# Kernel optimization log

Hardware: AMD Instinct MI355X
Metric: run time of the kernel (lower is better)

The kernel has to match this reference:

```python
import jax, jax.numpy as jnp
import numpy as np

B, W, F = 64, 128, 64          # batch, window (node feat dim), n_features (nodes)
H, OUTW = 4, 128               # num_heads, out window size
NEG_SLOPE = 0.2                # LeakyReLU negative slope (alpha)


def setup_inputs() -> dict:
    key = jax.random.key(0)
    ks = jax.random.split(key, 6)
    scale_in = 1.0 / np.sqrt(W)
    scale_a = 1.0 / np.sqrt(OUTW)
    return {
        "x": jax.random.normal(ks[0], (B, W, F), dtype=jnp.float32),
        "W_src": jax.random.normal(ks[1], (H * OUTW, W), dtype=jnp.float32) * scale_in,
        "b_src": jnp.zeros((H * OUTW,), dtype=jnp.float32),
        "W_dst": jax.random.normal(ks[2], (H * OUTW, W), dtype=jnp.float32) * scale_in,
        "b_dst": jnp.zeros((H * OUTW,), dtype=jnp.float32),
        "attn": jax.random.normal(ks[3], (H, OUTW), dtype=jnp.float32) * scale_a,
    }


def reference(x, W_src, b_src, W_dst, b_dst, attn):
    # x: [B, W, F] -> node features nf: [B, F, W] (F nodes, W-dim features)
    nf = jnp.transpose(x, (0, 2, 1))
    b, f, w = nf.shape
    h, outw = attn.shape
    # GATv2 separate source/destination projections (share_weights=False)
    fs = (nf @ W_src.T + b_src).reshape(b, f, h, outw)  # [B, F, H, outW]
    fd = (nf @ W_dst.T + b_dst).reshape(b, f, h, outw)
    # additive score over complete graph with self-loops: e[b,i,j,h,d]
    s = fs[:, :, None, :, :] + fd[:, None, :, :, :]      # [B, src, dst, H, outW]
    e = jnp.where(s >= 0, s, NEG_SLOPE * s)              # LeakyReLU
    scores = jnp.einsum('bijhd,hd->bhij', e, attn)       # [B, H, src, dst]
    # edge softmax: normalize over incoming edges (sources) per destination
    a = jax.nn.softmax(scores, axis=2)
    # weighted scatter-sum aggregation at destinations
    out = jnp.einsum('bhij,bihd->bjhd', a, fs)           # [B, F, H, outW]
    out = out.mean(axis=2)                               # mean over heads -> [B, F, outW]
    return jnp.transpose(out, (0, 2, 1))                 # [B, outW, F]
```

## Files before the change

### kernel.cpp

```cpp
#include <hip/hip_runtime.h>
#include <math.h>

#define BB 64
#define WW 128
#define FF 64
#define HH 4
#define OW 128


struct GemmRegion {
    float xq[64 * 68];
    float wq[2 * 128 * 68];
};
struct AttnRegion {
    float fsl[FF * 132];
    float fdl[FF * 132];
    float stT[FF * 68];
    float st2[FF * 68];
    float A6[OW], B4[OW];
    float redm[4 * 64];
    float invl[64];
    float xfer[256 * 36];
};
union SMem { GemmRegion g; AttnRegion a; };

__global__ void __launch_bounds__(512)
__attribute__((amdgpu_waves_per_eu(2, 2)))
gat_fused(
    const float* __restrict__ x,
    const float* __restrict__ Wsrc,
    const float* __restrict__ bsrc,
    const float* __restrict__ Wdst,
    const float* __restrict__ bdst,
    const float* __restrict__ attn,
    float* __restrict__ out)
{
    __shared__ __align__(16) SMem sm;
    __shared__ float bl[2 * 128];

    const int bx = blockIdx.x;
    const int h  = bx & 3;
    const int b  = bx >> 2;
    const int t  = threadIdx.x;

    const int m  = (t >> 7) & 1;
    const int ig = (t >> 4) & 7;
    const int dg = t & 15;
    const int i0 = ig * 8;

    if (t < 256) bl[t] = (t & 128 ? bdst : bsrc)[h * 128 + (t & 127)];

    float acc[8][8] = {};

    for (int kh = 0; kh < 2; ++kh) {
        if (kh) __syncthreads();
        #pragma unroll
        for (int p = 0; p < 2; ++p) {
            const int idx = p * 512 + t;
            const int k = idx >> 4, iq = idx & 15;
            *(float4*)&sm.g.xq[k * 68 + iq * 4] =
                *(const float4*)(x + ((size_t)b * WW + kh * 64 + k) * FF + iq * 4);
        }
        #pragma unroll
        for (int p = 0; p < 8; ++p) {
            const int idx = p * 512 + t;
            const int mm = idx >> 11, d = (idx >> 4) & 127, q = idx & 15;
            *(float4*)&sm.g.wq[(mm * 128 + d) * 68 + q * 4] =
                *(const float4*)((mm ? Wdst : Wsrc)
                                 + (size_t)(h * 128 + d) * WW + kh * 64 + q * 4);
        }
        __syncthreads();

        if (t < 256) {
            #pragma unroll 1
            for (int k0 = 0; k0 < 64; k0 += 4) {
                float4 wv[8];
                #pragma unroll
                for (int e = 0; e < 8; ++e)
                    wv[e] = *(const float4*)&sm.g.wq[(m * 128 + dg + 16 * e) * 68 + k0];
                #pragma unroll
                for (int kk = 0; kk < 4; ++kk) {
                    const float4 xa = *(const float4*)&sm.g.xq[(k0 + kk) * 68 + i0];
                    const float4 xb = *(const float4*)&sm.g.xq[(k0 + kk) * 68 + i0 + 4];
                    #pragma unroll
                    for (int e = 0; e < 8; ++e) {
                        const float wf = ((const float*)&wv[e])[kk];
                        acc[0][e] = fmaf(xa.x, wf, acc[0][e]);
                        acc[1][e] = fmaf(xa.y, wf, acc[1][e]);
                        acc[2][e] = fmaf(xa.z, wf, acc[2][e]);
                        acc[3][e] = fmaf(xa.w, wf, acc[3][e]);
                        acc[4][e] = fmaf(xb.x, wf, acc[4][e]);
                        acc[5][e] = fmaf(xb.y, wf, acc[5][e]);
                        acc[6][e] = fmaf(xb.z, wf, acc[6][e]);
                        acc[7][e] = fmaf(xb.w, wf, acc[7][e]);
                    }
                }
            }
        }
    }
    __syncthreads();

    if (t < 256) {
        float* dst = m ? sm.a.fdl : sm.a.fsl;
        #pragma unroll
        for (int e = 0; e < 8; ++e) {
            const int d = dg + 16 * e;
            const float bv = bl[m * 128 + d];
            #pragma unroll
            for (int ii = 0; ii < 8; ++ii)
                dst[(i0 + ii) * 132 + d] = acc[ii][e] + bv;
        }
    }
    if (t < 128) {
        const float av = attn[h * OW + t];
        sm.a.A6[t] = 0.6f * av;
        sm.a.B4[t] = 0.4f * av;
    }
    __syncthreads();

    if (t < 256) {
        const int i = t & 63, sel = t >> 6;
        const float* src = (sel < 2 ? sm.a.fsl : sm.a.fdl) + i * 132 + (sel & 1) * 64;
        const float* a6  = sm.a.A6 + (sel & 1) * 64;
        float s = 0.0f;
        #pragma unroll
        for (int c = 0; c < 16; ++c) {
            float4 fv = *(const float4*)&src[c * 4];
            float4 av = *(const float4*)&a6[c * 4];
            s = fmaf(fv.x, av.x, fmaf(fv.y, av.y, fmaf(fv.z, av.z, fmaf(fv.w, av.w, s))));
        }
        sm.a.redm[sel * 64 + i] = s;
    }
    __syncthreads();

    {
        const int dh  = t >> 8;
        const int rem = t & 255;
        const int iT  = rem & 15;
        const int j0D = (rem >> 4) * 4;
        float4 scq[4];
        scq[0] = scq[1] = scq[2] = scq[3] = float4{0.f, 0.f, 0.f, 0.f};
        const int cBase = dh * 16;
        #pragma unroll 4
        for (int c = 0; c < 16; ++c) {
            const int dd0 = (cBase + c) * 4;
            const float4 b4 = *(const float4*)&sm.a.B4[dd0];
            float4 fdv[4];
            #pragma unroll
            for (int jj = 0; jj < 4; ++jj)
                fdv[jj] = *(const float4*)&sm.a.fdl[(j0D + jj) * 132 + dd0];
            #pragma unroll
            for (int ii = 0; ii < 4; ++ii) {
                const float4 fsv =
                    *(const float4*)&sm.a.fsl[(iT + 16 * ii) * 132 + dd0];
                float* sc = (float*)&scq[ii];
                #pragma unroll
                for (int jj = 0; jj < 4; ++jj) {
                    float r = sc[jj];
                    r = fmaf(b4.x, fabsf(fsv.x + fdv[jj].x), r);
                    r = fmaf(b4.y, fabsf(fsv.y + fdv[jj].y), r);
                    r = fmaf(b4.z, fabsf(fsv.z + fdv[jj].z), r);
                    r = fmaf(b4.w, fabsf(fsv.w + fdv[jj].w), r);
                    sc[jj] = r;
                }
            }
        }
        if (dh) {
            #pragma unroll
            for (int ii = 0; ii < 4; ++ii)
                *(float4*)&sm.a.st2[(iT + 16 * ii) * 68 + j0D] = scq[ii];
        }
        __syncthreads();
        if (!dh) {
            float cdj[4];
            #pragma unroll
            for (int jj = 0; jj < 4; ++jj)
                cdj[jj] = sm.a.redm[128 + j0D + jj] + sm.a.redm[192 + j0D + jj];
            #pragma unroll
            for (int ii = 0; ii < 4; ++ii) {
                const int i = iT + 16 * ii;
                const float4 p2 = *(const float4*)&sm.a.st2[i * 68 + j0D];
                const float csl = sm.a.redm[i] + sm.a.redm[64 + i];
                const float* sc = (const float*)&scq[ii];
                const float* pp = (const float*)&p2;
                #pragma unroll
                for (int jj = 0; jj < 4; ++jj)
                    sm.a.stT[(j0D + jj) * 68 + i] = sc[jj] + pp[jj] + csl + cdj[jj];
            }
        }
    }
    __syncthreads();

    if (t < 64) {
        const int j = t;
        float* row = &sm.a.stT[j * 68];
        float4 rv[16];
        float mx = -3.0e38f;
        #pragma unroll
        for (int q = 0; q < 16; ++q) {
            rv[q] = *(const float4*)&row[q * 4];
            mx = fmaxf(mx, fmaxf(fmaxf(rv[q].x, rv[q].y), fmaxf(rv[q].z, rv[q].w)));
        }
        float s = 0.0f;
        #pragma unroll
        for (int q = 0; q < 16; ++q) {
            float4 e;
            e.x = __expf(rv[q].x - mx);
            e.y = __expf(rv[q].y - mx);
            e.z = __expf(rv[q].z - mx);
            e.w = __expf(rv[q].w - mx);
            s += e.x + e.y + e.z + e.w;
            *(float4*)&row[q * 4] = e;
        }
        sm.a.invl[j] = 0.25f / s;
    }
    __syncthreads();

    {
        const int ih  = t >> 8;
        const int rem = t & 255;
        const int jT  = rem & 15;
        const int dgF = rem >> 4;
        const int dF  = dgF * 4;
        const int iBase = ih * 32;

        float ag[4][8] = {};
        #pragma unroll 2
        for (int i2 = 0; i2 < 32; i2 += 4) {
            float4 pq[4];
            #pragma unroll
            for (int jj = 0; jj < 4; ++jj)
                pq[jj] = *(const float4*)&sm.a.stT[(jT + 16 * jj) * 68 + iBase + i2];
            #pragma unroll
            for (int u = 0; u < 4; ++u) {
                const int i = iBase + i2 + u;
                const float4 f0 = *(const float4*)&sm.a.fsl[i * 132 + dF];
                const float4 f1 = *(const float4*)&sm.a.fsl[i * 132 + dF + 64];
                #pragma unroll
                for (int jj = 0; jj < 4; ++jj) {
                    const float p = ((const float*)&pq[jj])[u];
                    ag[jj][0] = fmaf(p, f0.x, ag[jj][0]);
                    ag[jj][1] = fmaf(p, f0.y, ag[jj][1]);
                    ag[jj][2] = fmaf(p, f0.z, ag[jj][2]);
                    ag[jj][3] = fmaf(p, f0.w, ag[jj][3]);
                    ag[jj][4] = fmaf(p, f1.x, ag[jj][4]);
                    ag[jj][5] = fmaf(p, f1.y, ag[jj][5]);
                    ag[jj][6] = fmaf(p, f1.z, ag[jj][6]);
                    ag[jj][7] = fmaf(p, f1.w, ag[jj][7]);
                }
            }
        }

        if (ih) {
            #pragma unroll
            for (int jj = 0; jj < 4; ++jj) {
                float4 a0 = {ag[jj][0], ag[jj][1], ag[jj][2], ag[jj][3]};
                float4 a1 = {ag[jj][4], ag[jj][5], ag[jj][6], ag[jj][7]};
                *(float4*)&sm.a.xfer[rem * 36 + jj * 8]     = a0;
                *(float4*)&sm.a.xfer[rem * 36 + jj * 8 + 4] = a1;
            }
        }
        __syncthreads();
        if (!ih) {
            float* ob = out + (size_t)b * OW * FF;
            #pragma unroll
            for (int jj = 0; jj < 4; ++jj) {
                const float4 a0 = *(const float4*)&sm.a.xfer[rem * 36 + jj * 8];
                const float4 a1 = *(const float4*)&sm.a.xfer[rem * 36 + jj * 8 + 4];
                const float iv = sm.a.invl[jT + 16 * jj];
                const int j = jT + 16 * jj;
                atomicAdd(ob + (size_t)(dF + 0) * FF + j, (ag[jj][0] + a0.x) * iv);
                atomicAdd(ob + (size_t)(dF + 1) * FF + j, (ag[jj][1] + a0.y) * iv);
                atomicAdd(ob + (size_t)(dF + 2) * FF + j, (ag[jj][2] + a0.z) * iv);
                atomicAdd(ob + (size_t)(dF + 3) * FF + j, (ag[jj][3] + a0.w) * iv);
                atomicAdd(ob + (size_t)(dF + 64) * FF + j, (ag[jj][4] + a1.x) * iv);
                atomicAdd(ob + (size_t)(dF + 65) * FF + j, (ag[jj][5] + a1.y) * iv);
                atomicAdd(ob + (size_t)(dF + 66) * FF + j, (ag[jj][6] + a1.z) * iv);
                atomicAdd(ob + (size_t)(dF + 67) * FF + j, (ag[jj][7] + a1.w) * iv);
            }
        }
    }
}

extern "C" void kernel_launch(void* const* d_in, const int* in_sizes, int n_in,
                              void* d_out, int out_size, void* d_ws, size_t ws_size,
                              hipStream_t stream) {
    const float* x    = (const float*)d_in[0];
    const float* Wsrc = (const float*)d_in[1];
    const float* bsrc = (const float*)d_in[2];
    const float* Wdst = (const float*)d_in[3];
    const float* bdst = (const float*)d_in[4];
    const float* attn = (const float*)d_in[5];

    hipMemsetAsync(d_out, 0, (size_t)out_size, stream);
    gat_fused<<<BB * HH, 512, 0, stream>>>(x, Wsrc, bsrc, Wdst, bdst, attn,
                                           (float*)d_out);
}
```

Measured before the change: 102.6 us.

## Spread projection GEMM across all 512 threads and read x directly from global

```diff
diff --git a/kernel.cpp b/kernel.cpp
--- a/kernel.cpp
+++ b/kernel.cpp
@@ -9,7 +9,6 @@
 
 
 struct GemmRegion {
-    float xq[64 * 68];
     float wq[2 * 128 * 68];
 };
 struct AttnRegion {
@@ -43,24 +42,19 @@
     const int b  = bx >> 2;
     const int t  = threadIdx.x;
 
-    const int m  = (t >> 7) & 1;
-    const int ig = (t >> 4) & 7;
+    const int m  = t >> 8;
+    const int ig = (t >> 4) & 15;
     const int dg = t & 15;
-    const int i0 = ig * 8;
+    const int i0 = ig * 4;
 
     if (t < 256) bl[t] = (t & 128 ? bdst : bsrc)[h * 128 + (t & 127)];
 
-    float acc[8][8] = {};
+    const float* xb = x + (size_t)b * (WW * FF);
+
+    float acc[4][8] = {};
 
     for (int kh = 0; kh < 2; ++kh) {
         if (kh) __syncthreads();
-        #pragma unroll
-        for (int p = 0; p < 2; ++p) {
-            const int idx = p * 512 + t;
-            const int k = idx >> 4, iq = idx & 15;
-            *(float4*)&sm.g.xq[k * 68 + iq * 4] =
-                *(const float4*)(x + ((size_t)b * WW + kh * 64 + k) * FF + iq * 4);
-        }
         #pragma unroll
         for (int p = 0; p < 8; ++p) {
             const int idx = p * 512 + t;
@@ -71,43 +65,37 @@
         }
         __syncthreads();
 
-        if (t < 256) {
-            #pragma unroll 1
-            for (int k0 = 0; k0 < 64; k0 += 4) {
-                float4 wv[8];
-                #pragma unroll
-                for (int e = 0; e < 8; ++e)
-                    wv[e] = *(const float4*)&sm.g.wq[(m * 128 + dg + 16 * e) * 68 + k0];
-                #pragma unroll
-                for (int kk = 0; kk < 4; ++kk) {
-                    const float4 xa = *(const float4*)&sm.g.xq[(k0 + kk) * 68 + i0];
-                    const float4 xb = *(const float4*)&sm.g.xq[(k0 + kk) * 68 + i0 + 4];
-                    #pragma unroll
-                    for (int e = 0; e < 8; ++e) {
-                        const float wf = ((const float*)&wv[e])[kk];
-                        acc[0][e] = fmaf(xa.x, wf, acc[0][e]);
-                        acc[1][e] = fmaf(xa.y, wf, acc[1][e]);
-                        acc[2][e] = fmaf(xa.z, wf, acc[2][e]);
-                        acc[3][e] = fmaf(xa.w, wf, acc[3][e]);
-                        acc[4][e] = fmaf(xb.x, wf, acc[4][e]);
-                        acc[5][e] = fmaf(xb.y, wf, acc[5][e]);
-                        acc[6][e] = fmaf(xb.z, wf, acc[6][e]);
-                        acc[7][e] = fmaf(xb.w, wf, acc[7][e]);
-                    }
+        const float* xk = xb + (size_t)(kh * 64) * FF + i0;
+        #pragma unroll 1
+        for (int k0 = 0; k0 < 64; k0 += 4) {
+            float4 wv[8];
+            #pragma unroll
+            for (int e = 0; e < 8; ++e)
+                wv[e] = *(const float4*)&sm.g.wq[(m * 128 + dg + 16 * e) * 68 + k0];
+            #pragma unroll
+            for (int kk = 0; kk < 4; ++kk) {
+                const float4 xv = *(const float4*)(xk + (size_t)(k0 + kk) * FF);
+                #pragma unroll
+                for (int e = 0; e < 8; ++e) {
+                    const float wf = ((const float*)&wv[e])[kk];
+                    acc[0][e] = fmaf(xv.x, wf, acc[0][e]);
+                    acc[1][e] = fmaf(xv.y, wf, acc[1][e]);
+                    acc[2][e] = fmaf(xv.z, wf, acc[2][e]);
+                    acc[3][e] = fmaf(xv.w, wf, acc[3][e]);
                 }
             }
         }
     }
     __syncthreads();
 
-    if (t < 256) {
+    {
         float* dst = m ? sm.a.fdl : sm.a.fsl;
         #pragma unroll
         for (int e = 0; e < 8; ++e) {
             const int d = dg + 16 * e;
             const float bv = bl[m * 128 + d];
             #pragma unroll
-            for (int ii = 0; ii < 8; ++ii)
+            for (int ii = 0; ii < 4; ++ii)
                 dst[(i0 + ii) * 132 + d] = acc[ii][e] + bv;
         }
     }
```

Measured after the change: 101.1 us. Within noise of the previous version (-1.5%).
